# Performance work log

Measured on AMD Instinct MI355X. Metric: run time of the kernel, lower is better.

The kernel has to match this reference:

```python
import math
import jax, jax.numpy as jnp
import numpy as np

N_HEADS = 16
D_KV = 64
NUM_BUCKETS = 32
MAX_DISTANCE = 128


def _relative_position_bucket(relative_position, num_buckets=NUM_BUCKETS, max_distance=MAX_DISTANCE):
    # bidirectional=True (encoder)
    num_buckets //= 2
    n = -relative_position
    ret = (n < 0).astype(jnp.int32) * num_buckets
    n = jnp.abs(n)
    max_exact = num_buckets // 2
    is_small = n < max_exact
    val_if_large = max_exact + (
        jnp.log(jnp.maximum(n, 1).astype(jnp.float32) / max_exact)
        / math.log(max_distance / max_exact)
        * (num_buckets - max_exact)
    ).astype(jnp.int32)
    val_if_large = jnp.minimum(val_if_large, num_buckets - 1)
    return ret + jnp.where(is_small, n, val_if_large)


def setup_inputs() -> dict:
    key = jax.random.key(0)
    ks = jax.random.split(key, 6)
    B, S, D = 2, 2048, 1024
    scale = 0.02  # keep pre-softmax logits in a sane range
    return {
        "x": jax.random.normal(ks[0], (B, S, D), dtype=jnp.float32),
        "Wq": jax.random.normal(ks[1], (D, N_HEADS * D_KV), dtype=jnp.float32) * scale,
        "Wk": jax.random.normal(ks[2], (D, N_HEADS * D_KV), dtype=jnp.float32) * scale,
        "Wv": jax.random.normal(ks[3], (D, N_HEADS * D_KV), dtype=jnp.float32) * scale,
        "Wo": jax.random.normal(ks[4], (N_HEADS * D_KV, D), dtype=jnp.float32) * scale,
        "rel_emb": jax.random.normal(ks[5], (NUM_BUCKETS, N_HEADS), dtype=jnp.float32) * scale,
    }


def reference(x, Wq, Wk, Wv, Wo, rel_emb):
    B, S, D = x.shape
    H, Dk = N_HEADS, D_KV

    def shape(t):  # [B,S,H*Dk] -> [B,H,S,Dk]
        return t.reshape(B, S, H, Dk).transpose(0, 2, 1, 3)

    q = shape(x @ Wq)
    k = shape(x @ Wk)
    v = shape(x @ Wv)

    # NOTE: T5 attention has NO 1/sqrt(d) scaling.
    scores = jnp.einsum("bhqd,bhkd->bhqk", q, k)

    # relative position bias: [1, H, S, S]
    ctx_pos = jnp.arange(S)[:, None]
    mem_pos = jnp.arange(S)[None, :]
    rp_bucket = _relative_position_bucket(mem_pos - ctx_pos)  # [S, S]
    position_bias = rel_emb[rp_bucket].transpose(2, 0, 1)[None]  # [1,H,S,S]

    weights = jax.nn.softmax(scores + position_bias, axis=-1)
    context = jnp.einsum("bhqk,bhkd->bhqd", weights, v)
    context = context.transpose(0, 2, 1, 3).reshape(B, S, H * Dk)
    return context @ Wo
```

## Files before the change

kernel.cpp:

```cpp
#include <hip/hip_runtime.h>
#include <math.h>

typedef unsigned short u16;
typedef unsigned int u32;
typedef __attribute__((ext_vector_type(8))) short bf16x8_t;
typedef __attribute__((ext_vector_type(4))) float f32x4_t;
typedef __attribute__((ext_vector_type(16))) float f32x16_t;

#define S_LEN  2048
#define NH     16
#define DK     64
#define DMODEL 1024
#define MROWS  4096
#define LOG2E  1.44269504088896f

__device__ inline u16 f2b(float f) {
  union { float f; u32 u; } c; c.f = f;
  u32 u = c.u;
  return (u16)((u + 0x7fffu + ((u >> 16) & 1u)) >> 16);
}

__device__ __forceinline__ float fexp2(float x) {
#if __has_builtin(__builtin_amdgcn_exp2f)
  return __builtin_amdgcn_exp2f(x);
#else
  return exp2f(x);
#endif
}

__device__ __forceinline__ u32 cvtpk(float lo, float hi) {
  u32 r;
  asm("v_cvt_pk_bf16_f32 %0, %1, %2" : "=v"(r) : "v"(lo), "v"(hi));
  return r;
}

__device__ __forceinline__ void plswap(u32 &x, u32 &y) {
  asm("v_permlane32_swap_b32 %0, %1" : "+v"(x), "+v"(y));
}

__device__ __forceinline__ void stage16(const u16* gp_lane, u16* lds_base) {
#if __has_builtin(__builtin_amdgcn_global_load_lds)
  __builtin_amdgcn_global_load_lds((const __attribute__((address_space(1))) u32*)gp_lane,
                                   (__attribute__((address_space(3))) u32*)lds_base, 16, 0, 0);
#else
  *(uint4*)(lds_base + (threadIdx.x & 63) * 8) = *(const uint4*)gp_lane;
#endif
}

__global__ void prep_kernel(const float* __restrict__ x,
                            const float* __restrict__ Wq, const float* __restrict__ Wk,
                            const float* __restrict__ Wv, const float* __restrict__ Wo,
                            const float* __restrict__ rel,
                            u16* __restrict__ xb, u16* __restrict__ Wall,
                            u16* __restrict__ Wto, float* __restrict__ btab) {
  __shared__ float tile[32][33];
  const int bid = blockIdx.x, t = threadIdx.x;
  if (bid < 4096) {
    int i = (bid * 256 + t) * 4;
    float4 v = *(const float4*)(x + i);
    ushort4 o;
    o.x = f2b(v.x); o.y = f2b(v.y); o.z = f2b(v.z); o.w = f2b(v.w);
    *(ushort4*)(xb + i) = o;
  } else if (bid < 8192) {
    int bid2 = bid - 4096;
    int z = bid2 >> 10, rem = bid2 & 1023;
    const float* W; u16* Wt;
    switch (z) {
      case 0: W = Wq; Wt = Wall; break;
      case 1: W = Wk; Wt = Wall + (size_t)DMODEL * DMODEL; break;
      case 2: W = Wv; Wt = Wall + (size_t)2 * DMODEL * DMODEL; break;
      default: W = Wo; Wt = Wto; break;
    }
    int bc = (rem & 31) * 32, br = (rem >> 5) * 32;
    int tx = t & 31, ty = t >> 5;
    #pragma unroll
    for (int yy = 0; yy < 32; yy += 8)
      tile[ty + yy][tx] = W[(size_t)(br + ty + yy) * DMODEL + bc + tx];
    __syncthreads();
    #pragma unroll
    for (int yy = 0; yy < 32; yy += 8)
      Wt[(size_t)(bc + ty + yy) * DMODEL + br + tx] = f2b(tile[tx][ty + yy]);
  } else {
    int idx = (bid - 8192) * 256 + t;
    if (idx < NH * 4095) {
      int h = idx / 4095;
      int dpos = idx - h * 4095;
      int delta = dpos - 2047;
      int ret = (delta > 0) ? 16 : 0;
      int n = delta < 0 ? -delta : delta;
      int bucket;
      if (n < 8) {
        bucket = ret + n;
      } else {
        float vf = logf((float)n * 0.125f) / 2.7725887222397811f * 8.0f;
        int vil = 8 + (int)vf;
        bucket = ret + (vil < 15 ? vil : 15);
      }
      btab[idx] = (rel[bucket * NH + h] - 16.0f) * LOG2E;
    }
  }
}

#define GSTR 56
template <int MODE>
__global__ __launch_bounds__(256) void gemm128_kernel(const u16* __restrict__ A,
                                                      const u16* __restrict__ Bt,
                                                      float* __restrict__ C,
                                                      u16* __restrict__ q16,
                                                      u16* __restrict__ k16,
                                                      u16* __restrict__ vt16) {
  constexpr int ABSZ = (MODE == 1) ? 4608 : 128 * GSTR;
  constexpr int FSTR = (MODE == 1) ? 32 : GSTR;
  __shared__ __align__(16) u16 As[ABSZ];
  __shared__ __align__(16) u16 Bs[ABSZ];
  const int t = threadIdx.x, w = t >> 6, l = t & 63;
  const int c = l & 15, quad = l >> 4;
  const int m0 = blockIdx.x * 128, n0 = blockIdx.y * 128;
  const int wm = (w & 1) * 64, wn = (w >> 1) * 64;

  f32x4_t acc[16] = {};

  if constexpr (MODE == 1) {
    const int sr = l >> 2;
    const int k8 = (l & 3) * 8;
    const u16* Ag0 = A  + (size_t)(m0 + w * 32 + sr) * DMODEL + k8;
    const u16* Ag1 = Ag0 + (size_t)16 * DMODEL;
    const u16* Bg0 = Bt + (size_t)(n0 + w * 32 + sr) * DMODEL + k8;
    const u16* Bg1 = Bg0 + (size_t)16 * DMODEL;
    u16* Al = As + w * 1024;
    u16* Bl = Bs + w * 1024;
    for (int k0 = 0; k0 < DMODEL; k0 += 32) {
      __syncthreads();
      stage16(Ag0 + k0, Al);
      stage16(Ag1 + k0, Al + 512);
      stage16(Bg0 + k0, Bl);
      stage16(Bg1 + k0, Bl + 512);
      __syncthreads();
      bf16x8_t af[4], bfr[4];
      #pragma unroll
      for (int i = 0; i < 4; ++i) {
        af[i]  = *(const bf16x8_t*)(As + (wm + i * 16 + c) * FSTR + quad * 8);
        bfr[i] = *(const bf16x8_t*)(Bs + (wn + i * 16 + c) * FSTR + quad * 8);
      }
      #pragma unroll
      for (int mt = 0; mt < 4; ++mt)
        #pragma unroll
        for (int nt = 0; nt < 4; ++nt)
          acc[mt * 4 + nt] = __builtin_amdgcn_mfma_f32_16x16x32_bf16(af[mt], bfr[nt], acc[mt * 4 + nt], 0, 0, 0);
    }
  } else {
    const int sr = t >> 2;
    const int k8 = (t & 3) * 8;
    const u16* Ag0 = A  + (size_t)(m0 + sr) * DMODEL + k8;
    const u16* Ag1 = Ag0 + (size_t)64 * DMODEL;
    const u16* Bg0 = Bt + (size_t)(n0 + sr) * DMODEL + k8;
    const u16* Bg1 = Bg0 + (size_t)64 * DMODEL;
    u16* Al0 = As + sr * GSTR + k8;
    u16* Al1 = Al0 + 64 * GSTR;
    u16* Bl0 = Bs + sr * GSTR + k8;
    u16* Bl1 = Bl0 + 64 * GSTR;

    uint4 a0 = *(const uint4*)Ag0, a1 = *(const uint4*)Ag1;
    uint4 b0 = *(const uint4*)Bg0, b1 = *(const uint4*)Bg1;
    for (int k0 = 0; k0 < DMODEL; k0 += 32) {
      __syncthreads();
      *(uint4*)Al0 = a0; *(uint4*)Al1 = a1;
      *(uint4*)Bl0 = b0; *(uint4*)Bl1 = b1;
      __syncthreads();
      if (k0 + 32 < DMODEL) {
        a0 = *(const uint4*)(Ag0 + k0 + 32);
        a1 = *(const uint4*)(Ag1 + k0 + 32);
        b0 = *(const uint4*)(Bg0 + k0 + 32);
        b1 = *(const uint4*)(Bg1 + k0 + 32);
      }
      bf16x8_t af[4], bfr[4];
      #pragma unroll
      for (int i = 0; i < 4; ++i) {
        af[i]  = *(const bf16x8_t*)(As + (wm + i * 16 + c) * FSTR + quad * 8);
        bfr[i] = *(const bf16x8_t*)(Bs + (wn + i * 16 + c) * FSTR + quad * 8);
      }
      #pragma unroll
      for (int mt = 0; mt < 4; ++mt)
        #pragma unroll
        for (int nt = 0; nt < 4; ++nt)
          acc[mt * 4 + nt] = __builtin_amdgcn_mfma_f32_16x16x32_bf16(af[mt], bfr[nt], acc[mt * 4 + nt], 0, 0, 0);
    }
  }

  if constexpr (MODE == 0) {
    #pragma unroll
    for (int mt = 0; mt < 4; ++mt) {
      int grow0 = m0 + wm + mt * 16 + quad * 4;
      #pragma unroll
      for (int nt = 0; nt < 4; ++nt) {
        int gcol = n0 + wn + nt * 16 + c;
        #pragma unroll
        for (int r = 0; r < 4; ++r)
          C[(size_t)(grow0 + r) * DMODEL + gcol] = acc[mt * 4 + nt][r];
      }
    }
  } else {
    const int whichblk = n0 >> 10;
    if (whichblk == 2) {
      #pragma unroll
      for (int mt = 0; mt < 4; ++mt) {
        int grow0 = m0 + wm + mt * 16 + quad * 4;
        int b = grow0 >> 11, s0 = grow0 & 2047;
        #pragma unroll
        for (int nt = 0; nt < 4; ++nt) {
          int cc = (n0 + wn + nt * 16 + c) & 1023;
          int hh = cc >> 6, dk = cc & 63;
          f32x4_t v4 = acc[mt * 4 + nt];
          ushort4 o;
          o.x = f2b(v4[0]); o.y = f2b(v4[1]); o.z = f2b(v4[2]); o.w = f2b(v4[3]);
          *(ushort4*)(vt16 + (((size_t)(b * NH + hh)) * DK + dk) * S_LEN + s0) = o;
        }
      }
    } else {
      u16* tb = (w & 1) ? Bs : As;
      const int base_mw = m0 + wm;
      const int bb = base_mw >> 11, s0g = base_mw & 2047;
      const int cc = (n0 + wn) & 1023;
      const int hh = cc >> 6;
      u16* qk = (whichblk == 0 ? q16 : k16) + (((size_t)(bb * NH + hh)) * S_LEN + s0g) * DK;
      __syncthreads();
      #pragma unroll
      for (int round = 0; round < 2; ++round) {
        if ((w >> 1) == round) {
          #pragma unroll
          for (int mt = 0; mt < 4; ++mt)
            #pragma unroll
            for (int nt = 0; nt < 4; ++nt)
              #pragma unroll
              for (int r = 0; r < 4; ++r)
                tb[(mt * 16 + quad * 4 + r) * 72 + nt * 16 + c] = f2b(acc[mt * 4 + nt][r]);
          #pragma unroll
          for (int i = 0; i < 8; ++i) {
            int lrow = i * 8 + (l >> 3);
            int chk = l & 7;
            uint4 vv = *(const uint4*)(tb + lrow * 72 + chk * 8);
            *(uint4*)(qk + (size_t)lrow * DK + chk * 8) = vv;
          }
        }
        __syncthreads();
      }
    }
  }
}

#define ASTR 72
__global__ __launch_bounds__(512, 4) void attn_mfma_kernel(const u16* __restrict__ q,
                                                           const u16* __restrict__ k,
                                                           const u16* __restrict__ vt,
                                                           const float* __restrict__ btab,
                                                           u16* __restrict__ ctx) {
  __shared__ __align__(16) u16 Ks[64 * ASTR];
  __shared__ __align__(16) u16 Vts[64 * ASTR];
  __shared__ float band[192];
  __shared__ float Ored[4][64][33];
  __shared__ float lpx[4][32];

  const int t = threadIdx.x;
  const int w = t >> 6, l = t & 63;
  const int c32 = l & 31, h32 = l >> 5;
  const int grp = w >> 1, kh = w & 1;
  const int bh = blockIdx.y;
  const int h = bh & (NH - 1), b = bh >> 4;
  const int q0 = blockIdx.x * 128;

  const u16* qb = q + (size_t)bh * S_LEN * DK;
  const u16* kb = k + (size_t)bh * S_LEN * DK;
  const u16* vb = vt + (size_t)bh * DK * S_LEN;
  const float* btp = btab + h * 4095 + (2047 - 127 - q0);

  bf16x8_t qfrag[4];
  {
    const u16* qp = qb + (size_t)(q0 + grp * 32 + c32) * DK + h32 * 8;
    qfrag[0] = *(const bf16x8_t*)(qp);
    qfrag[1] = *(const bf16x8_t*)(qp + 16);
    qfrag[2] = *(const bf16x8_t*)(qp + 32);
    qfrag[3] = *(const bf16x8_t*)(qp + 48);
  }

  float lp = 0.f;
  f32x16_t O0 = {}, O1 = {};

  const int srow = t >> 3;
  const int sc8 = (t & 7) * 8;
  const u16* kg = kb + (size_t)srow * DK + sc8;
  const u16* vg = vb + (size_t)srow * S_LEN + sc8;
  u16* Kl = Ks + srow * ASTR + sc8;
  u16* Vl = Vts + srow * ASTR + sc8;

  uint4 kr = *(const uint4*)kg;
  uint4 vr = *(const uint4*)vg;
  float br = (t < 192) ? btp[t] : 0.f;

  const int krow = kh * 32 + c32;
  const int bndc = 127 + kh * 32 + 4 * h32 - grp * 32 - c32;

  for (int kt = 0; kt < S_LEN; kt += 64) {
    const int D = kt - q0;
    const bool far = (D >= 256) || (D <= -192);
    *(uint4*)Kl = kr;
    *(uint4*)Vl = vr;
    if (t < 192) band[t] = br;
    __syncthreads();
    if (kt + 64 < S_LEN) {
      kr = *(const uint4*)(kg + (size_t)(kt + 64) * DK);
      vr = *(const uint4*)(vg + (kt + 64));
      br = (t < 192) ? btp[kt + 64 + t] : 0.f;
    }

    f32x16_t s4 = {};
    __builtin_amdgcn_s_setprio(1);
    #pragma unroll
    for (int kb4 = 0; kb4 < 4; ++kb4) {
      bf16x8_t kf = *(const bf16x8_t*)(Ks + krow * ASTR + kb4 * 16 + h32 * 8);
      s4 = __builtin_amdgcn_mfma_f32_32x32x16_bf16(kf, qfrag[kb4], s4, 0, 0, 0);
    }
    __builtin_amdgcn_s_setprio(0);

    float p[16];
    if (far) {
      const float bfc = band[127];
      #pragma unroll
      for (int r = 0; r < 16; ++r)
        p[r] = fexp2(fmaf(s4[r], LOG2E, bfc));
    } else {
      #pragma unroll
      for (int r = 0; r < 16; ++r)
        p[r] = fexp2(fmaf(s4[r], LOG2E, band[bndc + (r & 3) + 8 * (r >> 2)]));
    }
    #pragma unroll
    for (int r = 0; r < 16; ++r)
      lp += p[r];

    union PW { u32 wds[4]; bf16x8_t v; } pa0, pa1;
    {
      u32 x, y;
      x = cvtpk(p[0], p[1]);  y = cvtpk(p[4], p[5]);   plswap(x, y);
      pa0.wds[0] = x; pa0.wds[2] = y;
      x = cvtpk(p[2], p[3]);  y = cvtpk(p[6], p[7]);   plswap(x, y);
      pa0.wds[1] = x; pa0.wds[3] = y;
      x = cvtpk(p[8], p[9]);  y = cvtpk(p[12], p[13]); plswap(x, y);
      pa1.wds[0] = x; pa1.wds[2] = y;
      x = cvtpk(p[10], p[11]); y = cvtpk(p[14], p[15]); plswap(x, y);
      pa1.wds[1] = x; pa1.wds[3] = y;
    }

    __builtin_amdgcn_s_setprio(1);
    {
      bf16x8_t vf00 = *(const bf16x8_t*)(Vts + (c32)      * ASTR + kh * 32 + h32 * 8);
      bf16x8_t vf01 = *(const bf16x8_t*)(Vts + (32 + c32) * ASTR + kh * 32 + h32 * 8);
      O0 = __builtin_amdgcn_mfma_f32_32x32x16_bf16(pa0.v, vf00, O0, 0, 0, 0);
      O1 = __builtin_amdgcn_mfma_f32_32x32x16_bf16(pa0.v, vf01, O1, 0, 0, 0);
      bf16x8_t vf10 = *(const bf16x8_t*)(Vts + (c32)      * ASTR + kh * 32 + 16 + h32 * 8);
      bf16x8_t vf11 = *(const bf16x8_t*)(Vts + (32 + c32) * ASTR + kh * 32 + 16 + h32 * 8);
      O0 = __builtin_amdgcn_mfma_f32_32x32x16_bf16(pa1.v, vf10, O0, 0, 0, 0);
      O1 = __builtin_amdgcn_mfma_f32_32x32x16_bf16(pa1.v, vf11, O1, 0, 0, 0);
    }
    __builtin_amdgcn_s_setprio(0);
    __syncthreads();
  }

  lp += __shfl_xor(lp, 32, 64);

  if (kh == 1) {
    #pragma unroll
    for (int r = 0; r < 16; ++r) {
      Ored[grp][l][r]      = O0[r];
      Ored[grp][l][16 + r] = O1[r];
    }
    if (l < 32) lpx[grp][l] = lp;
  }
  __syncthreads();
  if (kh == 0) {
    lp += lpx[grp][c32];
    float rv = 1.0f / lp;
    #pragma unroll
    for (int r = 0; r < 16; ++r) {
      int qr = (r & 3) + 8 * (r >> 2) + 4 * h32;
      float inv = __shfl(rv, qr, 64);
      float o0 = O0[r] + Ored[grp][l][r];
      float o1 = O1[r] + Ored[grp][l][16 + r];
      int s = q0 + grp * 32 + qr;
      u16* cp = ctx + ((size_t)(b * S_LEN + s)) * DMODEL + h * DK;
      cp[c32]      = f2b(o0 * inv);
      cp[32 + c32] = f2b(o1 * inv);
    }
  }
}

extern "C" void kernel_launch(void* const* d_in, const int* in_sizes, int n_in,
                              void* d_out, int out_size, void* d_ws, size_t ws_size,
                              hipStream_t stream) {
  const float* x   = (const float*)d_in[0];
  const float* Wq  = (const float*)d_in[1];
  const float* Wk  = (const float*)d_in[2];
  const float* Wv  = (const float*)d_in[3];
  const float* Wo  = (const float*)d_in[4];
  const float* rel = (const float*)d_in[5];
  float* out = (float*)d_out;

  char* ws = (char*)d_ws;
  size_t off = 0;
  auto carve = [&](size_t bytes) -> char* {
    char* p = ws + off;
    off += (bytes + 255) & ~(size_t)255;
    return p;
  };
  u16*   xb   = (u16*)  carve((size_t)MROWS * DMODEL * 2);
  u16*   Wall = (u16*)  carve((size_t)3 * DMODEL * DMODEL * 2);
  u16*   Wto  = (u16*)  carve((size_t)DMODEL * DMODEL * 2);
  u16*   qb16 = (u16*)  carve((size_t)4194304 * 2);
  u16*   kb16 = (u16*)  carve((size_t)4194304 * 2);
  u16*   vt16 = (u16*)  carve((size_t)4194304 * 2);
  float* btab = (float*)carve(((size_t)NH * 4095 + 256) * 4);
  u16*   ctxb = (u16*)  carve((size_t)4194304 * 2);

  prep_kernel<<<8448, 256, 0, stream>>>(x, Wq, Wk, Wv, Wo, rel, xb, Wall, Wto, btab);

  dim3 qkvgrid(32, 24);
  gemm128_kernel<1><<<qkvgrid, 256, 0, stream>>>(xb, Wall, nullptr, qb16, kb16, vt16);

  dim3 agrid(S_LEN / 128, 32);
  attn_mfma_kernel<<<agrid, 512, 0, stream>>>(qb16, kb16, vt16, btab, ctxb);

  dim3 ogrid(32, 8);
  gemm128_kernel<0><<<ogrid, 256, 0, stream>>>(ctxb, Wto, out, nullptr, nullptr, nullptr);
}
```

Before: 186.1 us.

## Double-buffer K/V tiles in attention and halve query tile per block

```diff
diff --git a/kernel.cpp b/kernel.cpp
--- a/kernel.cpp
+++ b/kernel.cpp
@@ -249,16 +249,15 @@
 }
 
 #define ASTR 72
-__global__ __launch_bounds__(512, 4) void attn_mfma_kernel(const u16* __restrict__ q,
-                                                           const u16* __restrict__ k,
-                                                           const u16* __restrict__ vt,
-                                                           const float* __restrict__ btab,
-                                                           u16* __restrict__ ctx) {
-  __shared__ __align__(16) u16 Ks[64 * ASTR];
-  __shared__ __align__(16) u16 Vts[64 * ASTR];
-  __shared__ float band[192];
-  __shared__ float Ored[4][64][33];
-  __shared__ float lpx[4][32];
+__global__ __launch_bounds__(256) void attn_mfma_kernel(const u16* __restrict__ q,
+                                                        const u16* __restrict__ k,
+                                                        const u16* __restrict__ vt,
+                                                        const float* __restrict__ btab,
+                                                        u16* __restrict__ ctx) {
+  __shared__ __align__(16) u16 Ks[2][64 * ASTR];
+  __shared__ __align__(16) u16 Vts[2][64 * ASTR];
+  __shared__ float band[2][192];
+  __shared__ float lpx[2][32];
 
   const int t = threadIdx.x;
   const int w = t >> 6, l = t & 63;
@@ -266,7 +265,7 @@
   const int grp = w >> 1, kh = w & 1;
   const int bh = blockIdx.y;
   const int h = bh & (NH - 1), b = bh >> 4;
-  const int q0 = blockIdx.x * 128;
+  const int q0 = blockIdx.x * 64;
 
   const u16* qb = q + (size_t)bh * S_LEN * DK;
   const u16* kb = k + (size_t)bh * S_LEN * DK;
@@ -287,50 +286,72 @@
 
   const int srow = t >> 3;
   const int sc8 = (t & 7) * 8;
-  const u16* kg = kb + (size_t)srow * DK + sc8;
-  const u16* vg = vb + (size_t)srow * S_LEN + sc8;
-  u16* Kl = Ks + srow * ASTR + sc8;
-  u16* Vl = Vts + srow * ASTR + sc8;
-
-  uint4 kr = *(const uint4*)kg;
-  uint4 vr = *(const uint4*)vg;
-  float br = (t < 192) ? btp[t] : 0.f;
+  const u16* kg0 = kb + (size_t)srow * DK + sc8;
+  const u16* kg1 = kg0 + (size_t)32 * DK;
+  const u16* vg0 = vb + (size_t)srow * S_LEN + sc8;
+  const u16* vg1 = vg0 + (size_t)32 * S_LEN;
+  const int so0 = srow * ASTR + sc8;
+  const int so1 = (srow + 32) * ASTR + sc8;
 
   const int krow = kh * 32 + c32;
   const int bndc = 127 + kh * 32 + 4 * h32 - grp * 32 - c32;
 
+  {
+    uint4 a0 = *(const uint4*)kg0, a1 = *(const uint4*)kg1;
+    uint4 b0 = *(const uint4*)vg0, b1 = *(const uint4*)vg1;
+    *(uint4*)(Ks[0] + so0) = a0;  *(uint4*)(Ks[0] + so1) = a1;
+    *(uint4*)(Vts[0] + so0) = b0; *(uint4*)(Vts[0] + so1) = b1;
+    if (t < 192) band[0][t] = btp[t];
+  }
+  uint4 kr0 = *(const uint4*)(kg0 + (size_t)64 * DK);
+  uint4 kr1 = *(const uint4*)(kg1 + (size_t)64 * DK);
+  uint4 vr0 = *(const uint4*)(vg0 + 64);
+  uint4 vr1 = *(const uint4*)(vg1 + 64);
+  float br = (t < 192) ? btp[64 + t] : 0.f;
+  __syncthreads();
+
   for (int kt = 0; kt < S_LEN; kt += 64) {
+    const int cur = (kt >> 6) & 1;
     const int D = kt - q0;
-    const bool far = (D >= 256) || (D <= -192);
-    *(uint4*)Kl = kr;
-    *(uint4*)Vl = vr;
-    if (t < 192) band[t] = br;
-    __syncthreads();
+    const bool far = (D >= 192) || (D <= -192);
+
     if (kt + 64 < S_LEN) {
-      kr = *(const uint4*)(kg + (size_t)(kt + 64) * DK);
-      vr = *(const uint4*)(vg + (kt + 64));
-      br = (t < 192) ? btp[kt + 64 + t] : 0.f;
-    }
+      u16* Kn = Ks[cur ^ 1]; u16* Vn = Vts[cur ^ 1];
+      *(uint4*)(Kn + so0) = kr0;  *(uint4*)(Kn + so1) = kr1;
+      *(uint4*)(Vn + so0) = vr0;  *(uint4*)(Vn + so1) = vr1;
+      if (t < 192) band[cur ^ 1][t] = br;
+      if (kt + 128 < S_LEN) {
+        kr0 = *(const uint4*)(kg0 + (size_t)(kt + 128) * DK);
+        kr1 = *(const uint4*)(kg1 + (size_t)(kt + 128) * DK);
+        vr0 = *(const uint4*)(vg0 + (kt + 128));
+        vr1 = *(const uint4*)(vg1 + (kt + 128));
+        br = (t < 192) ? btp[kt + 128 + t] : 0.f;
+      }
+    }
+
+    const u16* Kc = Ks[cur];
+    const u16* Vc = Vts[cur];
+    const float* bandc = band[cur];
 
     f32x16_t s4 = {};
     __builtin_amdgcn_s_setprio(1);
     #pragma unroll
     for (int kb4 = 0; kb4 < 4; ++kb4) {
-      bf16x8_t kf = *(const bf16x8_t*)(Ks + krow * ASTR + kb4 * 16 + h32 * 8);
+      bf16x8_t kf = *(const bf16x8_t*)(Kc + krow * ASTR + kb4 * 16 + h32 * 8);
       s4 = __builtin_amdgcn_mfma_f32_32x32x16_bf16(kf, qfrag[kb4], s4, 0, 0, 0);
     }
     __builtin_amdgcn_s_setprio(0);
 
     float p[16];
     if (far) {
-      const float bfc = band[127];
+      const float bfc = bandc[127];
       #pragma unroll
       for (int r = 0; r < 16; ++r)
         p[r] = fexp2(fmaf(s4[r], LOG2E, bfc));
     } else {
       #pragma unroll
       for (int r = 0; r < 16; ++r)
-        p[r] = fexp2(fmaf(s4[r], LOG2E, band[bndc + (r & 3) + 8 * (r >> 2)]));
+        p[r] = fexp2(fmaf(s4[r], LOG2E, bandc[bndc + (r & 3) + 8 * (r >> 2)]));
     }
     #pragma unroll
     for (int r = 0; r < 16; ++r)
@@ -339,11 +360,11 @@
     union PW { u32 wds[4]; bf16x8_t v; } pa0, pa1;
     {
       u32 x, y;
-      x = cvtpk(p[0], p[1]);  y = cvtpk(p[4], p[5]);   plswap(x, y);
+      x = cvtpk(p[0], p[1]);   y = cvtpk(p[4], p[5]);   plswap(x, y);
       pa0.wds[0] = x; pa0.wds[2] = y;
-      x = cvtpk(p[2], p[3]);  y = cvtpk(p[6], p[7]);   plswap(x, y);
+      x = cvtpk(p[2], p[3]);   y = cvtpk(p[6], p[7]);   plswap(x, y);
       pa0.wds[1] = x; pa0.wds[3] = y;
-      x = cvtpk(p[8], p[9]);  y = cvtpk(p[12], p[13]); plswap(x, y);
+      x = cvtpk(p[8], p[9]);   y = cvtpk(p[12], p[13]); plswap(x, y);
       pa1.wds[0] = x; pa1.wds[2] = y;
       x = cvtpk(p[10], p[11]); y = cvtpk(p[14], p[15]); plswap(x, y);
       pa1.wds[1] = x; pa1.wds[3] = y;
@@ -351,12 +372,12 @@
 
     __builtin_amdgcn_s_setprio(1);
     {
-      bf16x8_t vf00 = *(const bf16x8_t*)(Vts + (c32)      * ASTR + kh * 32 + h32 * 8);
-      bf16x8_t vf01 = *(const bf16x8_t*)(Vts + (32 + c32) * ASTR + kh * 32 + h32 * 8);
+      bf16x8_t vf00 = *(const bf16x8_t*)(Vc + (c32)      * ASTR + kh * 32 + h32 * 8);
+      bf16x8_t vf01 = *(const bf16x8_t*)(Vc + (32 + c32) * ASTR + kh * 32 + h32 * 8);
       O0 = __builtin_amdgcn_mfma_f32_32x32x16_bf16(pa0.v, vf00, O0, 0, 0, 0);
       O1 = __builtin_amdgcn_mfma_f32_32x32x16_bf16(pa0.v, vf01, O1, 0, 0, 0);
-      bf16x8_t vf10 = *(const bf16x8_t*)(Vts + (c32)      * ASTR + kh * 32 + 16 + h32 * 8);
-      bf16x8_t vf11 = *(const bf16x8_t*)(Vts + (32 + c32) * ASTR + kh * 32 + 16 + h32 * 8);
+      bf16x8_t vf10 = *(const bf16x8_t*)(Vc + (c32)      * ASTR + kh * 32 + 16 + h32 * 8);
+      bf16x8_t vf11 = *(const bf16x8_t*)(Vc + (32 + c32) * ASTR + kh * 32 + 16 + h32 * 8);
       O0 = __builtin_amdgcn_mfma_f32_32x32x16_bf16(pa1.v, vf10, O0, 0, 0, 0);
       O1 = __builtin_amdgcn_mfma_f32_32x32x16_bf16(pa1.v, vf11, O1, 0, 0, 0);
     }
@@ -365,6 +386,7 @@
   }
 
   lp += __shfl_xor(lp, 32, 64);
+  float (*Ored)[64][33] = (float (*)[64][33])(&Ks[0][0]);
 
   if (kh == 1) {
     #pragma unroll
@@ -424,8 +446,8 @@
   dim3 qkvgrid(32, 24);
   gemm128_kernel<1><<<qkvgrid, 256, 0, stream>>>(xb, Wall, nullptr, qb16, kb16, vt16);
 
-  dim3 agrid(S_LEN / 128, 32);
-  attn_mfma_kernel<<<agrid, 512, 0, stream>>>(qb16, kb16, vt16, btab, ctxb);
+  dim3 agrid(S_LEN / 64, 32);
+  attn_mfma_kernel<<<agrid, 256, 0, stream>>>(qb16, kb16, vt16, btab, ctxb);
 
   dim3 ogrid(32, 8);
   gemm128_kernel<0><<<ogrid, 256, 0, stream>>>(ctxb, Wto, out, nullptr, nullptr, nullptr);
```

Result: slower. 206.5 us (+10.9%).

## Double attention KV tile to 128 keys, alias reduction smem, swizzle block order

Applied to the files above, without the earlier changes.

```diff
diff --git a/kernel.cpp b/kernel.cpp
--- a/kernel.cpp
+++ b/kernel.cpp
@@ -248,25 +248,29 @@
   }
 }
 
-#define ASTR 72
+#define KSTR 72
+#define VSTR 136
 __global__ __launch_bounds__(512, 4) void attn_mfma_kernel(const u16* __restrict__ q,
                                                            const u16* __restrict__ k,
                                                            const u16* __restrict__ vt,
                                                            const float* __restrict__ btab,
                                                            u16* __restrict__ ctx) {
-  __shared__ __align__(16) u16 Ks[64 * ASTR];
-  __shared__ __align__(16) u16 Vts[64 * ASTR];
-  __shared__ float band[192];
-  __shared__ float Ored[4][64][33];
-  __shared__ float lpx[4][32];
+  __shared__ __align__(16) char smem[37376];
+  u16*   Ks   = (u16*)smem;
+  u16*   Vts  = (u16*)(smem + 18432);
+  float* band = (float*)(smem + 35840);
+  float* lpx  = (float*)(smem + 36864);
 
   const int t = threadIdx.x;
   const int w = t >> 6, l = t & 63;
   const int c32 = l & 31, h32 = l >> 5;
   const int grp = w >> 1, kh = w & 1;
-  const int bh = blockIdx.y;
+
+  const int orig = blockIdx.x;
+  const int swz = (orig & 7) * 64 + (orig >> 3);
+  const int bh = swz >> 4;
+  const int q0 = (swz & 15) * 128;
   const int h = bh & (NH - 1), b = bh >> 4;
-  const int q0 = blockIdx.x * 128;
 
   const u16* qb = q + (size_t)bh * S_LEN * DK;
   const u16* kb = k + (size_t)bh * S_LEN * DK;
@@ -285,86 +289,131 @@
   float lp = 0.f;
   f32x16_t O0 = {}, O1 = {};
 
-  const int srow = t >> 3;
-  const int sc8 = (t & 7) * 8;
-  const u16* kg = kb + (size_t)srow * DK + sc8;
-  const u16* vg = vb + (size_t)srow * S_LEN + sc8;
-  u16* Kl = Ks + srow * ASTR + sc8;
-  u16* Vl = Vts + srow * ASTR + sc8;
-
-  uint4 kr = *(const uint4*)kg;
-  uint4 vr = *(const uint4*)vg;
-  float br = (t < 192) ? btp[t] : 0.f;
-
-  const int krow = kh * 32 + c32;
-  const int bndc = 127 + kh * 32 + 4 * h32 - grp * 32 - c32;
-
-  for (int kt = 0; kt < S_LEN; kt += 64) {
+  const int ksr = t >> 2;
+  const int ksc = (t & 3) * 8;
+  const u16* kgp = kb + (size_t)ksr * DK + ksc;
+  u16* Kl = Ks + ksr * KSTR + ksc;
+  const int vsr = t >> 3;
+  const int vsc = (t & 7) * 8;
+  const u16* vgp = vb + (size_t)vsr * S_LEN + vsc;
+  u16* Vl = Vts + vsr * VSTR + vsc;
+
+  uint4 kr0 = *(const uint4*)kgp;
+  uint4 kr1 = *(const uint4*)(kgp + 32);
+  uint4 vr0 = *(const uint4*)vgp;
+  uint4 vr1 = *(const uint4*)(vgp + 64);
+  float br = (t < 256) ? btp[t] : 0.f;
+
+  const int krA = (kh * 64 + c32) * KSTR + h32 * 8;
+  const int bndcA = 127 + kh * 64 + 4 * h32 - grp * 32 - c32;
+
+  for (int kt = 0; kt < S_LEN; kt += 128) {
+    *(uint4*)Kl = kr0;        *(uint4*)(Kl + 32) = kr1;
+    *(uint4*)Vl = vr0;        *(uint4*)(Vl + 64) = vr1;
+    if (t < 256) band[t] = br;
+    __syncthreads();
+    if (kt + 128 < S_LEN) {
+      kr0 = *(const uint4*)(kgp + (size_t)(kt + 128) * DK);
+      kr1 = *(const uint4*)(kgp + (size_t)(kt + 128) * DK + 32);
+      vr0 = *(const uint4*)(vgp + (kt + 128));
+      vr1 = *(const uint4*)(vgp + (kt + 128) + 64);
+      br = (t < 256) ? btp[kt + 128 + t] : 0.f;
+    }
     const int D = kt - q0;
-    const bool far = (D >= 256) || (D <= -192);
-    *(uint4*)Kl = kr;
-    *(uint4*)Vl = vr;
-    if (t < 192) band[t] = br;
-    __syncthreads();
-    if (kt + 64 < S_LEN) {
-      kr = *(const uint4*)(kg + (size_t)(kt + 64) * DK);
-      vr = *(const uint4*)(vg + (kt + 64));
-      br = (t < 192) ? btp[kt + 64 + t] : 0.f;
-    }
-
-    f32x16_t s4 = {};
+    const bool far = (D >= 256) || (D <= -256);
+
+    f32x16_t sA = {}, sB = {};
     __builtin_amdgcn_s_setprio(1);
     #pragma unroll
     for (int kb4 = 0; kb4 < 4; ++kb4) {
-      bf16x8_t kf = *(const bf16x8_t*)(Ks + krow * ASTR + kb4 * 16 + h32 * 8);
-      s4 = __builtin_amdgcn_mfma_f32_32x32x16_bf16(kf, qfrag[kb4], s4, 0, 0, 0);
+      bf16x8_t kfA = *(const bf16x8_t*)(Ks + krA + kb4 * 16);
+      sA = __builtin_amdgcn_mfma_f32_32x32x16_bf16(kfA, qfrag[kb4], sA, 0, 0, 0);
+    }
+    #pragma unroll
+    for (int kb4 = 0; kb4 < 4; ++kb4) {
+      bf16x8_t kfB = *(const bf16x8_t*)(Ks + krA + 32 * KSTR + kb4 * 16);
+      sB = __builtin_amdgcn_mfma_f32_32x32x16_bf16(kfB, qfrag[kb4], sB, 0, 0, 0);
     }
     __builtin_amdgcn_s_setprio(0);
 
-    float p[16];
-    if (far) {
-      const float bfc = band[127];
+    const float bfc = band[127];
+
+    {
+      float p[16];
+      if (far) {
+        #pragma unroll
+        for (int r = 0; r < 16; ++r)
+          p[r] = fexp2(fmaf(sA[r], LOG2E, bfc));
+      } else {
+        #pragma unroll
+        for (int r = 0; r < 16; ++r)
+          p[r] = fexp2(fmaf(sA[r], LOG2E, band[bndcA + (r & 3) + 8 * (r >> 2)]));
+      }
       #pragma unroll
       for (int r = 0; r < 16; ++r)
-        p[r] = fexp2(fmaf(s4[r], LOG2E, bfc));
-    } else {
-      #pragma unroll
-      for (int r = 0; r < 16; ++r)
-        p[r] = fexp2(fmaf(s4[r], LOG2E, band[bndc + (r & 3) + 8 * (r >> 2)]));
-    }
-    #pragma unroll
-    for (int r = 0; r < 16; ++r)
-      lp += p[r];
-
-    union PW { u32 wds[4]; bf16x8_t v; } pa0, pa1;
-    {
+        lp += p[r];
+      union PW { u32 wds[4]; bf16x8_t v; } pa0, pa1;
       u32 x, y;
-      x = cvtpk(p[0], p[1]);  y = cvtpk(p[4], p[5]);   plswap(x, y);
+      x = cvtpk(p[0], p[1]);   y = cvtpk(p[4], p[5]);   plswap(x, y);
       pa0.wds[0] = x; pa0.wds[2] = y;
-      x = cvtpk(p[2], p[3]);  y = cvtpk(p[6], p[7]);   plswap(x, y);
+      x = cvtpk(p[2], p[3]);   y = cvtpk(p[6], p[7]);   plswap(x, y);
       pa0.wds[1] = x; pa0.wds[3] = y;
-      x = cvtpk(p[8], p[9]);  y = cvtpk(p[12], p[13]); plswap(x, y);
+      x = cvtpk(p[8], p[9]);   y = cvtpk(p[12], p[13]); plswap(x, y);
       pa1.wds[0] = x; pa1.wds[2] = y;
       x = cvtpk(p[10], p[11]); y = cvtpk(p[14], p[15]); plswap(x, y);
       pa1.wds[1] = x; pa1.wds[3] = y;
-    }
-
-    __builtin_amdgcn_s_setprio(1);
-    {
-      bf16x8_t vf00 = *(const bf16x8_t*)(Vts + (c32)      * ASTR + kh * 32 + h32 * 8);
-      bf16x8_t vf01 = *(const bf16x8_t*)(Vts + (32 + c32) * ASTR + kh * 32 + h32 * 8);
+      __builtin_amdgcn_s_setprio(1);
+      bf16x8_t vf00 = *(const bf16x8_t*)(Vts + (c32)      * VSTR + kh * 64 + h32 * 8);
+      bf16x8_t vf01 = *(const bf16x8_t*)(Vts + (32 + c32) * VSTR + kh * 64 + h32 * 8);
       O0 = __builtin_amdgcn_mfma_f32_32x32x16_bf16(pa0.v, vf00, O0, 0, 0, 0);
       O1 = __builtin_amdgcn_mfma_f32_32x32x16_bf16(pa0.v, vf01, O1, 0, 0, 0);
-      bf16x8_t vf10 = *(const bf16x8_t*)(Vts + (c32)      * ASTR + kh * 32 + 16 + h32 * 8);
-      bf16x8_t vf11 = *(const bf16x8_t*)(Vts + (32 + c32) * ASTR + kh * 32 + 16 + h32 * 8);
+      bf16x8_t vf10 = *(const bf16x8_t*)(Vts + (c32)      * VSTR + kh * 64 + 16 + h32 * 8);
+      bf16x8_t vf11 = *(const bf16x8_t*)(Vts + (32 + c32) * VSTR + kh * 64 + 16 + h32 * 8);
       O0 = __builtin_amdgcn_mfma_f32_32x32x16_bf16(pa1.v, vf10, O0, 0, 0, 0);
       O1 = __builtin_amdgcn_mfma_f32_32x32x16_bf16(pa1.v, vf11, O1, 0, 0, 0);
-    }
-    __builtin_amdgcn_s_setprio(0);
+      __builtin_amdgcn_s_setprio(0);
+    }
+
+    {
+      float p[16];
+      if (far) {
+        #pragma unroll
+        for (int r = 0; r < 16; ++r)
+          p[r] = fexp2(fmaf(sB[r], LOG2E, bfc));
+      } else {
+        #pragma unroll
+        for (int r = 0; r < 16; ++r)
+          p[r] = fexp2(fmaf(sB[r], LOG2E, band[bndcA + 32 + (r & 3) + 8 * (r >> 2)]));
+      }
+      #pragma unroll
+      for (int r = 0; r < 16; ++r)
+        lp += p[r];
+      union PW { u32 wds[4]; bf16x8_t v; } pa0, pa1;
+      u32 x, y;
+      x = cvtpk(p[0], p[1]);   y = cvtpk(p[4], p[5]);   plswap(x, y);
+      pa0.wds[0] = x; pa0.wds[2] = y;
+      x = cvtpk(p[2], p[3]);   y = cvtpk(p[6], p[7]);   plswap(x, y);
+      pa0.wds[1] = x; pa0.wds[3] = y;
+      x = cvtpk(p[8], p[9]);   y = cvtpk(p[12], p[13]); plswap(x, y);
+      pa1.wds[0] = x; pa1.wds[2] = y;
+      x = cvtpk(p[10], p[11]); y = cvtpk(p[14], p[15]); plswap(x, y);
+      pa1.wds[1] = x; pa1.wds[3] = y;
+      __builtin_amdgcn_s_setprio(1);
+      bf16x8_t vf00 = *(const bf16x8_t*)(Vts + (c32)      * VSTR + kh * 64 + 32 + h32 * 8);
+      bf16x8_t vf01 = *(const bf16x8_t*)(Vts + (32 + c32) * VSTR + kh * 64 + 32 + h32 * 8);
+      O0 = __builtin_amdgcn_mfma_f32_32x32x16_bf16(pa0.v, vf00, O0, 0, 0, 0);
+      O1 = __builtin_amdgcn_mfma_f32_32x32x16_bf16(pa0.v, vf01, O1, 0, 0, 0);
+      bf16x8_t vf10 = *(const bf16x8_t*)(Vts + (c32)      * VSTR + kh * 64 + 48 + h32 * 8);
+      bf16x8_t vf11 = *(const bf16x8_t*)(Vts + (32 + c32) * VSTR + kh * 64 + 48 + h32 * 8);
+      O0 = __builtin_amdgcn_mfma_f32_32x32x16_bf16(pa1.v, vf10, O0, 0, 0, 0);
+      O1 = __builtin_amdgcn_mfma_f32_32x32x16_bf16(pa1.v, vf11, O1, 0, 0, 0);
+      __builtin_amdgcn_s_setprio(0);
+    }
     __syncthreads();
   }
 
   lp += __shfl_xor(lp, 32, 64);
+  float (*Ored)[64][33] = (float (*)[64][33])smem;
 
   if (kh == 1) {
     #pragma unroll
@@ -372,11 +421,11 @@
       Ored[grp][l][r]      = O0[r];
       Ored[grp][l][16 + r] = O1[r];
     }
-    if (l < 32) lpx[grp][l] = lp;
+    if (l < 32) lpx[grp * 32 + l] = lp;
   }
   __syncthreads();
   if (kh == 0) {
-    lp += lpx[grp][c32];
+    lp += lpx[grp * 32 + c32];
     float rv = 1.0f / lp;
     #pragma unroll
     for (int r = 0; r < 16; ++r) {
@@ -424,8 +473,7 @@
   dim3 qkvgrid(32, 24);
   gemm128_kernel<1><<<qkvgrid, 256, 0, stream>>>(xb, Wall, nullptr, qb16, kb16, vt16);
 
-  dim3 agrid(S_LEN / 128, 32);
-  attn_mfma_kernel<<<agrid, 512, 0, stream>>>(qb16, kb16, vt16, btab, ctxb);
+  attn_mfma_kernel<<<512, 512, 0, stream>>>(qb16, kb16, vt16, btab, ctxb);
 
   dim3 ogrid(32, 8);
   gemm128_kernel<0><<<ogrid, 256, 0, stream>>>(ctxb, Wto, out, nullptr, nullptr, nullptr);
```

Result: no change. 185.1 us (-0.5%).
